# Kernel optimization log

Measured on AMD Instinct MI355X. Metric: run time of the kernel, lower is better.

The kernel has to match this reference:

```python
import jax, jax.numpy as jnp
import numpy as np

BATCH, CHANNELS, WINDOW, N_PATCHES = 16, 64, 200, 30
D_MODEL = 256
HIDDEN = D_MODEL // 2  # 128


def setup_inputs() -> dict:
    key = jax.random.key(0)
    ks = jax.random.split(key, 7)
    s = 1.0 / np.sqrt(HIDDEN)
    return {
        "x": jax.random.normal(ks[0], (BATCH, CHANNELS, WINDOW, N_PATCHES), dtype=jnp.float32),
        "W_ih": jax.random.normal(ks[1], (4 * HIDDEN, CHANNELS), dtype=jnp.float32) * s,
        "W_hh": jax.random.normal(ks[2], (4 * HIDDEN, HIDDEN), dtype=jnp.float32) * s,
        "b_ih": jax.random.normal(ks[3], (4 * HIDDEN,), dtype=jnp.float32) * s,
        "b_hh": jax.random.normal(ks[4], (4 * HIDDEN,), dtype=jnp.float32) * s,
        "W_fc": jax.random.normal(ks[5], (CHANNELS, HIDDEN), dtype=jnp.float32) * s,
        "b_fc": jax.random.normal(ks[6], (CHANNELS,), dtype=jnp.float32) * s,
    }


def _lstm_last_h(x_seq, W_ih, W_hh, b_ih, b_hh):
    # x_seq: (N, T, C) -> final hidden state (N, H). PyTorch gate order: i, f, g, o.
    N = x_seq.shape[0]
    H = W_hh.shape[1]
    # Precompute input contribution for all timesteps: (N, T, 4H)
    xg = jnp.einsum('ntc,gc->ntg', x_seq, W_ih) + b_ih + b_hh
    xg_t = jnp.swapaxes(xg, 0, 1)  # (T, N, 4H)

    def step(carry, xt):
        h, c = carry
        gates = xt + h @ W_hh.T  # (N, 4H)
        i, f, g, o = jnp.split(gates, 4, axis=-1)
        i = jax.nn.sigmoid(i)
        f = jax.nn.sigmoid(f)
        g = jnp.tanh(g)
        o = jax.nn.sigmoid(o)
        c = f * c + i * g
        h = o * jnp.tanh(c)
        return (h, c), None

    h0 = jnp.zeros((N, H), dtype=x_seq.dtype)
    c0 = jnp.zeros((N, H), dtype=x_seq.dtype)
    (h_T, _), _ = jax.lax.scan(step, (h0, c0), xg_t)
    return h_T


def reference(x, W_ih, W_hh, b_ih, b_hh, W_fc, b_fc):
    batch, channels, window, n_patches = x.shape
    # (B, C, T, P) -> (B, P, T, C) -> (B*P, T, C): each patch is an LSTM sequence
    x_flat = jnp.transpose(x, (0, 3, 2, 1)).reshape(batch * n_patches, window, channels)
    h_last = _lstm_last_h(x_flat, W_ih, W_hh, b_ih, b_hh)  # (B*P, H)
    out = h_last @ W_fc.T + b_fc  # (B*P, C)
    return out.reshape(batch, n_patches, channels)
```

## Files before the change

kernel.cpp:

```cpp
#include <hip/hip_runtime.h>

#define BATCH 16
#define CH    64
#define TLEN  200
#define NP    30
#define HID   128
#define NSEQ  (BATCH * NP)
#define HXP   136
#define XBP   72
#define XGW   520

typedef _Float16 half8 __attribute__((ext_vector_type(8)));
typedef float    f32x4 __attribute__((ext_vector_type(4)));

__device__ __forceinline__ float sigm_fast(float x) {
    return __builtin_amdgcn_rcpf(1.0f + __expf(-x));
}
__device__ __forceinline__ float tanh_fast(float x) {
    return 1.0f - 2.0f * __builtin_amdgcn_rcpf(__expf(2.0f * x) + 1.0f);
}
__device__ __forceinline__ half8 cvt8(float4 a, float4 b) {
    return (half8){(_Float16)a.x,(_Float16)a.y,(_Float16)a.z,(_Float16)a.w,
                   (_Float16)b.x,(_Float16)b.y,(_Float16)b.z,(_Float16)b.w};
}

#define MFMA16(A,B,C) __builtin_amdgcn_mfma_f32_16x16x32_f16((A),(B),(C),0,0,0)

__global__ __launch_bounds__(512, 2) void fused_lstm(
    const float* __restrict__ x, const float* __restrict__ W_ih,
    const float* __restrict__ W_hh, const float* __restrict__ b_ih,
    const float* __restrict__ b_hh, const float* __restrict__ W_fc,
    const float* __restrict__ b_fc, float* __restrict__ out)
{
    const int tid = threadIdx.x;
    const int w  = tid >> 6;
    const int l  = tid & 63;
    const int lr = l & 15;
    const int lq = l >> 4;

    const int blk  = blockIdx.x;
    const int pair = (blk & 7) * 30 + (blk >> 3);
    const int n0 = pair * 2;
    const int b0 = n0 / NP;
    const int p0 = n0 % NP;

    __shared__ __align__(16) _Float16 hx2[2][16][HXP];
    __shared__ __align__(16) _Float16 xbuf[2][16][XBP];
    __shared__ __align__(16) float    xgb[2][16 * XGW];

    half8 bhh[4][4];
    half8 bih[4][2];
    float biasx[4];
#pragma unroll
    for (int T = 0; T < 4; ++T) {
        const int g = 128*T + 16*w + lr;
        const float* rh = W_hh + (size_t)g * HID;
        const float* ri = W_ih + (size_t)g * CH;
#pragma unroll
        for (int kt = 0; kt < 4; ++kt) {
            const int k0 = 32*kt + 8*lq;
            bhh[T][kt] = cvt8(*(const float4*)(rh + k0), *(const float4*)(rh + k0 + 4));
        }
#pragma unroll
        for (int j = 0; j < 2; ++j) {
            const int k0 = 32*j + 8*lq;
            bih[T][j] = cvt8(*(const float4*)(ri + k0), *(const float4*)(ri + k0 + 4));
        }
        biasx[T] = b_ih[g] + b_hh[g];
    }

    for (int i = tid; i < (2*16*HXP)/2; i += 512) ((unsigned*)hx2)[i] = 0u;

    const bool isload = (l >= 32 && l < 48);
    int ls = 0, lc = 0;
    const float* xbase = nullptr;
    float xpend = 0.f;
    if (isload) {
        const int idx = w * 16 + (l - 32);
        ls = idx >> 6;
        lc = idx & 63;
        xbase = x + ((size_t)(b0 * CH + lc) * TLEN) * NP + p0 + ls;
#pragma unroll
        for (int u = 0; u < 16; ++u)
            xbuf[u >> 3][2*(u & 7) + ls][lc] = (_Float16)xbase[(size_t)u * NP];
        xpend = xbase[(size_t)16 * NP];
    }
    float cst = 0.f;
    const int hcol = 16*w + lr;
    __syncthreads();

#define XG_BURST(SB, TB) {                                                        \
        const _Float16* xr_ = &xbuf[SB][lr][8*lq];                                \
        half8 xf0_ = *(const half8*)xr_;                                          \
        half8 xf1_ = *(const half8*)(xr_ + 32);                                   \
        f32x4 g0_ = {biasx[0], biasx[0], biasx[0], biasx[0]};                     \
        f32x4 g1_ = {biasx[1], biasx[1], biasx[1], biasx[1]};                     \
        f32x4 g2_ = {biasx[2], biasx[2], biasx[2], biasx[2]};                     \
        f32x4 g3_ = {biasx[3], biasx[3], biasx[3], biasx[3]};                     \
        g0_ = MFMA16(xf0_, bih[0][0], g0_); g0_ = MFMA16(xf1_, bih[0][1], g0_);   \
        g1_ = MFMA16(xf0_, bih[1][0], g1_); g1_ = MFMA16(xf1_, bih[1][1], g1_);   \
        g2_ = MFMA16(xf0_, bih[2][0], g2_); g2_ = MFMA16(xf1_, bih[2][1], g2_);   \
        g3_ = MFMA16(xf0_, bih[3][0], g3_); g3_ = MFMA16(xf1_, bih[3][1], g3_);   \
        _Pragma("unroll") for (int r_ = 0; r_ < 4; ++r_) {                        \
            float* dst_ = &xgb[TB][(4*lq + r_) * XGW + hcol * 4];                 \
            *(f32x4*)dst_ = (f32x4){g0_[r_], g1_[r_], g2_[r_], g3_[r_]};          \
        } }

    XG_BURST(0, 0)
    __syncthreads();

#pragma unroll 1
    for (int p = 0; p < 25; ++p) {
        const int pe = p & 1;
#pragma unroll
        for (int k = 0; k < 8; ++k) {
            const int cur = k & 1;
            const int nxt = cur ^ 1;
            f32x4 xg4 = *(const f32x4*)&xgb[pe][(2*k + (lq & 1)) * XGW + hcol * 4];
            const _Float16* hr = &hx2[cur][lr][8*lq];
            half8 a0 = *(const half8*)(hr);
            half8 a1 = *(const half8*)(hr + 32);
            half8 a2 = *(const half8*)(hr + 64);
            half8 a3 = *(const half8*)(hr + 96);
            f32x4 ci = xg4;
            f32x4 cf = __builtin_shufflevector(xg4, xg4, 1, 1, 1, 1);
            f32x4 cg = __builtin_shufflevector(xg4, xg4, 2, 2, 2, 2);
            f32x4 co = __builtin_shufflevector(xg4, xg4, 3, 3, 3, 3);
            __builtin_amdgcn_s_setprio(1);
            ci = MFMA16(a0, bhh[0][0], ci); ci = MFMA16(a1, bhh[0][1], ci);
            ci = MFMA16(a2, bhh[0][2], ci); ci = MFMA16(a3, bhh[0][3], ci);
            cf = MFMA16(a0, bhh[1][0], cf); cf = MFMA16(a1, bhh[1][1], cf);
            cf = MFMA16(a2, bhh[1][2], cf); cf = MFMA16(a3, bhh[1][3], cf);
            cg = MFMA16(a0, bhh[2][0], cg); cg = MFMA16(a1, bhh[2][1], cg);
            cg = MFMA16(a2, bhh[2][2], cg); cg = MFMA16(a3, bhh[2][3], cg);
            float si = sigm_fast(ci[0]);
            float sf = sigm_fast(cf[0]);
            float tg = tanh_fast(cg[0]);
            float cnew = sf * cst + si * tg;
            co = MFMA16(a0, bhh[3][0], co); co = MFMA16(a1, bhh[3][1], co);
            co = MFMA16(a2, bhh[3][2], co); co = MFMA16(a3, bhh[3][3], co);
            __builtin_amdgcn_s_setprio(0);
            if (k == 0 && p < 24) XG_BURST(pe ^ 1, pe ^ 1)
            if (isload) {
                xbuf[pe][2*k + ls][lc] = (_Float16)xpend;
                int tq = 8*p + k + 17;
                tq = tq > TLEN - 1 ? TLEN - 1 : tq;
                xpend = xbase[(size_t)tq * NP];
            }
            float hv = sigm_fast(co[0]) * tanh_fast(cnew);
            cst = cnew;
            hx2[nxt][4*lq][hcol] = (_Float16)hv;
            __syncthreads();
        }
    }

    if (tid < 2 * CH) {
        const int s = tid >> 6, ch = tid & 63;
        const float* wf = W_fc + (size_t)ch * HID;
        float acc = b_fc[ch];
#pragma unroll
        for (int j8 = 0; j8 < 16; ++j8) {
            half8 hv = *(const half8*)&hx2[0][4*s][8 * j8];
            float4 w0 = *(const float4*)(wf + 8 * j8);
            float4 w1 = *(const float4*)(wf + 8 * j8 + 4);
            acc += w0.x * (float)hv[0] + w0.y * (float)hv[1]
                 + w0.z * (float)hv[2] + w0.w * (float)hv[3]
                 + w1.x * (float)hv[4] + w1.y * (float)hv[5]
                 + w1.z * (float)hv[6] + w1.w * (float)hv[7];
        }
        out[(size_t)(n0 + s) * CH + ch] = acc;
    }
}

extern "C" void kernel_launch(void* const* d_in, const int* in_sizes, int n_in,
                              void* d_out, int out_size, void* d_ws, size_t ws_size,
                              hipStream_t stream) {
    (void)in_sizes; (void)n_in; (void)out_size; (void)d_ws; (void)ws_size;
    fused_lstm<<<NSEQ / 2, 512, 0, stream>>>(
        (const float*)d_in[0], (const float*)d_in[1], (const float*)d_in[2],
        (const float*)d_in[3], (const float*)d_in[4], (const float*)d_in[5],
        (const float*)d_in[6], (float*)d_out);
}
```

Before: 193.4 us.

## Preload whole input sequence into LDS and add input gates after MFMA

Before the recurrence, the full per-block input sequence (all 200 timesteps, both sequences) is loaded into a large LDS buffer. This replaces the per-step streamed global loads that a subset of lanes issued inside the sequential loop, so the input-gate bursts read only from LDS. The recurrent MFMA accumulators now start from zero and the precomputed input gates are added afterwards, which takes the xg shared-memory read out of the MFMA dependency chain. The cost is a serial, poorly coalesced prologue load, plus a larger LDS footprint that likely limits the kernel to one block per CU.

```diff
diff --git a/kernel.cpp b/kernel.cpp
--- a/kernel.cpp
+++ b/kernel.cpp
@@ -7,7 +7,7 @@
 #define HID   128
 #define NSEQ  (BATCH * NP)
 #define HXP   136
-#define XBP   72
+#define XP    72
 #define XGW   520
 
 typedef _Float16 half8 __attribute__((ext_vector_type(8)));
@@ -45,7 +45,7 @@
     const int p0 = n0 % NP;
 
     __shared__ __align__(16) _Float16 hx2[2][16][HXP];
-    __shared__ __align__(16) _Float16 xbuf[2][16][XBP];
+    __shared__ __align__(16) _Float16 xlds[TLEN][2][XP];
     __shared__ __align__(16) float    xgb[2][16 * XGW];
 
     half8 bhh[4][4];
@@ -71,26 +71,19 @@
 
     for (int i = tid; i < (2*16*HXP)/2; i += 512) ((unsigned*)hx2)[i] = 0u;
 
-    const bool isload = (l >= 32 && l < 48);
-    int ls = 0, lc = 0;
-    const float* xbase = nullptr;
-    float xpend = 0.f;
-    if (isload) {
-        const int idx = w * 16 + (l - 32);
-        ls = idx >> 6;
-        lc = idx & 63;
-        xbase = x + ((size_t)(b0 * CH + lc) * TLEN) * NP + p0 + ls;
-#pragma unroll
-        for (int u = 0; u < 16; ++u)
-            xbuf[u >> 3][2*(u & 7) + ls][lc] = (_Float16)xbase[(size_t)u * NP];
-        xpend = xbase[(size_t)16 * NP];
+    for (int e = tid; e < CH * TLEN; e += 512) {
+        const int t = e % TLEN, c = e / TLEN;
+        const float* src = x + ((size_t)(b0 * CH + c) * TLEN + t) * NP + p0;
+        float2 v = *(const float2*)src;
+        xlds[t][0][c] = (_Float16)v.x;
+        xlds[t][1][c] = (_Float16)v.y;
     }
     float cst = 0.f;
     const int hcol = 16*w + lr;
     __syncthreads();
 
-#define XG_BURST(SB, TB) {                                                        \
-        const _Float16* xr_ = &xbuf[SB][lr][8*lq];                                \
+#define XG_BURST(P, TB) {                                                         \
+        const _Float16* xr_ = &xlds[8*(P) + (lr >> 1)][lr & 1][8*lq];             \
         half8 xf0_ = *(const half8*)xr_;                                          \
         half8 xf1_ = *(const half8*)(xr_ + 32);                                   \
         f32x4 g0_ = {biasx[0], biasx[0], biasx[0], biasx[0]};                     \
@@ -122,10 +115,8 @@
             half8 a1 = *(const half8*)(hr + 32);
             half8 a2 = *(const half8*)(hr + 64);
             half8 a3 = *(const half8*)(hr + 96);
-            f32x4 ci = xg4;
-            f32x4 cf = __builtin_shufflevector(xg4, xg4, 1, 1, 1, 1);
-            f32x4 cg = __builtin_shufflevector(xg4, xg4, 2, 2, 2, 2);
-            f32x4 co = __builtin_shufflevector(xg4, xg4, 3, 3, 3, 3);
+            f32x4 zz = {0.f, 0.f, 0.f, 0.f};
+            f32x4 ci = zz, cf = zz, cg = zz, co = zz;
             __builtin_amdgcn_s_setprio(1);
             ci = MFMA16(a0, bhh[0][0], ci); ci = MFMA16(a1, bhh[0][1], ci);
             ci = MFMA16(a2, bhh[0][2], ci); ci = MFMA16(a3, bhh[0][3], ci);
@@ -133,21 +124,15 @@
             cf = MFMA16(a2, bhh[1][2], cf); cf = MFMA16(a3, bhh[1][3], cf);
             cg = MFMA16(a0, bhh[2][0], cg); cg = MFMA16(a1, bhh[2][1], cg);
             cg = MFMA16(a2, bhh[2][2], cg); cg = MFMA16(a3, bhh[2][3], cg);
-            float si = sigm_fast(ci[0]);
-            float sf = sigm_fast(cf[0]);
-            float tg = tanh_fast(cg[0]);
+            float si = sigm_fast(ci[0] + xg4[0]);
+            float sf = sigm_fast(cf[0] + xg4[1]);
+            float tg = tanh_fast(cg[0] + xg4[2]);
             float cnew = sf * cst + si * tg;
             co = MFMA16(a0, bhh[3][0], co); co = MFMA16(a1, bhh[3][1], co);
             co = MFMA16(a2, bhh[3][2], co); co = MFMA16(a3, bhh[3][3], co);
             __builtin_amdgcn_s_setprio(0);
-            if (k == 0 && p < 24) XG_BURST(pe ^ 1, pe ^ 1)
-            if (isload) {
-                xbuf[pe][2*k + ls][lc] = (_Float16)xpend;
-                int tq = 8*p + k + 17;
-                tq = tq > TLEN - 1 ? TLEN - 1 : tq;
-                xpend = xbase[(size_t)tq * NP];
-            }
-            float hv = sigm_fast(co[0]) * tanh_fast(cnew);
+            if (k == 0 && p < 24) XG_BURST(p + 1, pe ^ 1)
+            float hv = sigm_fast(co[0] + xg4[3]) * tanh_fast(cnew);
             cst = cnew;
             hx2[nxt][4*lq][hcol] = (_Float16)hv;
             __syncthreads();
```

Measured after the change: 192.6 us. No clear change (-0.5%).
